# Kernel tuning notes

Measured on AMD Instinct MI355X. Metric: run time of the kernel, lower is better.

The kernel has to match this reference:

```python
import jax, jax.numpy as jnp
import numpy as np

EPS = 1e-12

def _l2norm(x):
    # F.normalize(p=2, dim=1) with eps clamp on the norm
    n = jnp.linalg.norm(x, axis=1, keepdims=True)
    return x / jnp.maximum(n, EPS)

def _xavier_uniform(key, shape, gain=1.414):
    fan_in, fan_out = shape[-1], shape[0]
    a = gain * np.sqrt(6.0 / (fan_in + fan_out))
    return jax.random.uniform(key, shape, jnp.float32, -a, a)

def setup_inputs() -> dict:
    NUM_ENT, NUM_REL, D, E, B = 100000, 500, 512, 150000, 4096
    key = jax.random.key(0)
    ks = jax.random.split(key, 12)
    heads = jax.random.randint(ks[0], (B, 1), 0, NUM_ENT)
    rels  = jax.random.randint(ks[1], (B, 1), 0, NUM_REL)
    tails = jax.random.randint(ks[2], (B, 1), 0, NUM_ENT)
    triples = jnp.concatenate([heads, rels, tails], axis=1)           # [B,3]
    node_list = jax.random.randint(ks[3], (2, E), 0, NUM_ENT)          # [2,E] (src,dst)
    edge_list = jax.random.randint(ks[4], (E,), 0, NUM_REL)            # [E] relation per edge
    return {
        "triples": triples,
        "node_list": node_list,
        "edge_list": edge_list,
        "ent_emb_init": jax.random.normal(ks[5], (NUM_ENT, D), jnp.float32),
        "rel_emb_init": jax.random.normal(ks[6], (NUM_REL, D), jnp.float32),
        "W_1": _xavier_uniform(ks[7], (D, D)),
        "W_a": _xavier_uniform(ks[8], (1, D)),
        "g_0": _xavier_uniform(ks[9], (1, D)),
        "W_E": _xavier_uniform(ks[10], (D, D)),
        "W_R": _xavier_uniform(ks[11], (D, D)),
    }

def reference(triples, node_list, edge_list, ent_emb_init, rel_emb_init,
              W_1, W_a, g_0, W_E, W_R):
    num_ent = ent_emb_init.shape[0]
    e0 = _l2norm(ent_emb_init)                      # normalized entity table [N,D]
    src, dst = node_list[0], node_list[1]
    h_i = e0[src]                                   # [E,D]
    h_j = e0[dst]                                   # [E,D]
    g_k = rel_emb_init[edge_list]                   # [E,D]

    # c_ijk = W_1 @ (h_j*g_k)^T  -> kept edge-major as [E,D]
    c = (h_j * g_k) @ W_1.T                         # [E,D]
    a = -jax.nn.leaky_relu((h_i * jnp.tanh(c)) @ W_a[0], 0.2)   # [E]
    c_base = (h_i * g_0) @ W_1.T                    # [E,D]
    a_base = -jax.nn.leaky_relu((h_i * jnp.tanh(c_base)) @ W_a[0], 0.2)  # [E]

    a_exp = jnp.exp(a)                              # [E]
    ab_exp = jnp.exp(a_base)                        # [E]

    # segment-softmax denominator: sum of edge exps per source node + baseline term
    a_exp_sum = jax.ops.segment_sum(a_exp[:, None], src, num_segments=num_ent)  # [N,1]
    # baseline exp depends only on src node -> duplicate scatter-set writes identical values
    ab_sorted = jnp.zeros_like(a_exp_sum).at[src].set(ab_exp[:, None])           # [N,1]
    denom = ab_sorted + a_exp_sum
    denom = jnp.where(denom == 0.0, EPS, denom)

    # weighted scatter-aggregate of messages (dropout omitted: eval-mode identity)
    ac = a_exp[:, None] * c                         # [E,D]
    ac_base = ab_exp[:, None] * c_base              # [E,D]
    a_new = jax.ops.segment_sum(ac, src, num_segments=num_ent)                   # [N,D]
    ab_new = jnp.zeros_like(a_new).at[src].set(ac_base)                          # [N,D]

    h_prime = jax.nn.elu((ab_new + a_new) / denom)  # [N,D]
    ent_new = _l2norm(e0 @ W_E + h_prime)           # [N,D]
    rel_new = rel_emb_init @ W_R                    # [R,D]

    head = ent_new[triples[:, 0]][:, None, :]       # [B,1,D]
    rel  = rel_new[triples[:, 1]][:, None, :]       # [B,1,D]
    tail = ent_new[triples[:, 2]][:, None, :]       # [B,1,D]
    return jnp.concatenate([head, rel, tail], axis=1)  # [B,3,D]
```

## Files before the change

kernel.cpp:

```cpp
#include <hip/hip_runtime.h>
#include <cmath>


#define DDIM 512
#define MAXM 65536
#define GBM 128
#define GBN 128

typedef __attribute__((ext_vector_type(8))) short short8;
typedef __attribute__((ext_vector_type(4))) float fv4;
typedef unsigned short u16;

__device__ __forceinline__ float elu1(float x) { return x > 0.f ? x : expm1f(x); }
__device__ __forceinline__ float sexp(float x) {
    float lr = x >= 0.f ? x : 0.2f * x;
    return expf(-lr);
}
__device__ __forceinline__ u16 f2bf(float x) {
    unsigned u = __float_as_uint(x);
    u += 0x7FFFu + ((u >> 16) & 1u);
    return (u16)(u >> 16);
}
__device__ __forceinline__ float bf2f(u16 h) {
    return __uint_as_float((unsigned)h << 16);
}
__device__ __forceinline__ void cvt8(const float* v, short8& h8, short8& l8) {
    #pragma unroll
    for (int i = 0; i < 8; i++) {
        u16 h = f2bf(v[i]);
        h8[i] = (short)h;
        l8[i] = (short)f2bf(v[i] - bf2f(h));
    }
}
__device__ __forceinline__ void gld16(const void* g, void* l) {
    __builtin_amdgcn_global_load_lds(
        (const __attribute__((address_space(1))) unsigned int*)g,
        (__attribute__((address_space(3))) unsigned int*)l,
        16, 0, 0);
}

__global__ __launch_bounds__(128)
void invnorm_sel_kernel(const float* __restrict__ emb, const int* __restrict__ slotNode,
                        const int* __restrict__ rowsL, const int* __restrict__ dstIdx,
                        const int* __restrict__ Mdev, int NS, float* __restrict__ invN)
{
    __shared__ float ws2[2];
    int total = NS + min(MAXM, *Mdev);
    int t = threadIdx.x;
    for (int q = blockIdx.x; q < total; q += gridDim.x) {
        int n = (q < NS) ? slotNode[q] : dstIdx[rowsL[q - NS]];
        float4 v = *(const float4*)(emb + (size_t)n * DDIM + t * 4);
        float s = v.x*v.x + v.y*v.y + v.z*v.z + v.w*v.w;
        #pragma unroll
        for (int off = 32; off > 0; off >>= 1) s += __shfl_down(s, off);
        if ((t & 63) == 0) ws2[t >> 6] = s;
        __syncthreads();
        if (t == 0) invN[n] = 1.f / fmaxf(sqrtf(ws2[0] + ws2[1]), 1e-12f);
        __syncthreads();
    }
}

__global__ __launch_bounds__(128)
void l2norm_kernel(float* __restrict__ data)
{
    int r = blockIdx.x, t = threadIdx.x;
    size_t o = (size_t)r * DDIM + t * 4;
    float4 v = *(const float4*)(data + o);
    float s = v.x*v.x + v.y*v.y + v.z*v.z + v.w*v.w;
    #pragma unroll
    for (int off = 32; off > 0; off >>= 1) s += __shfl_down(s, off);
    __shared__ float ws2[2];
    if ((t & 63) == 0) ws2[t >> 6] = s;
    __syncthreads();
    float inv = 1.f / fmaxf(sqrtf(ws2[0] + ws2[1]), 1e-12f);
    *(float4*)(data + o) = make_float4(v.x*inv, v.y*inv, v.z*inv, v.w*inv);
}

__global__ __launch_bounds__(256)
void transpose512_kernel(const float* __restrict__ in, float* __restrict__ out)
{
    __shared__ float tile[32][33];
    int bx = blockIdx.x & 15, by = blockIdx.x >> 4;
    int x = threadIdx.x & 31, y0 = (threadIdx.x >> 5) * 4;
    #pragma unroll
    for (int i = 0; i < 4; i++)
        tile[y0 + i][x] = in[(size_t)(by * 32 + y0 + i) * 512 + bx * 32 + x];
    __syncthreads();
    #pragma unroll
    for (int i = 0; i < 4; i++)
        out[(size_t)(bx * 32 + y0 + i) * 512 + by * 32 + x] = tile[x][y0 + i];
}

__global__ void hist_kernel(const int* __restrict__ src, int* __restrict__ cnt, int E)
{
    int e = blockIdx.x * 256 + threadIdx.x;
    if (e < E) atomicAdd(&cnt[src[e]], 1);
}

__global__ __launch_bounds__(1024)
void scan1_kernel(const int* __restrict__ in, int* __restrict__ out,
                  int* __restrict__ blockTot, int n)
{
    __shared__ int sh[1024];
    int t = threadIdx.x;
    int i = blockIdx.x * 1024 + t;
    int v = (i < n) ? in[i] : 0;
    sh[t] = v;
    __syncthreads();
    for (int off = 1; off < 1024; off <<= 1) {
        int x = (t >= off) ? sh[t - off] : 0;
        __syncthreads();
        sh[t] += x;
        __syncthreads();
    }
    if (i < n) out[i] = sh[t] - v;
    if (t == 1023) blockTot[blockIdx.x] = sh[1023];
}

__global__ __launch_bounds__(1024)
void scan2_kernel(const int* __restrict__ blockTot, int* __restrict__ blockOff,
                  int* __restrict__ outLast, int G)
{
    __shared__ int sh[1024];
    int t = threadIdx.x;
    int v = (t < G) ? blockTot[t] : 0;
    sh[t] = v;
    __syncthreads();
    for (int off = 1; off < 1024; off <<= 1) {
        int x = (t >= off) ? sh[t - off] : 0;
        __syncthreads();
        sh[t] += x;
        __syncthreads();
    }
    if (t < G) blockOff[t] = sh[t] - v;
    if (t == 1023) *outLast = sh[1023];
}

__global__ __launch_bounds__(1024)
void scan3_kernel(int* __restrict__ out, const int* __restrict__ blockOff, int n)
{
    int i = blockIdx.x * 1024 + threadIdx.x;
    if (i < n) out[i] += blockOff[blockIdx.x];
}

__global__ void bucket_kernel(const int* __restrict__ src, int* __restrict__ cursor,
                              int* __restrict__ edge_ids, int E)
{
    int e = blockIdx.x * 256 + threadIdx.x;
    if (e < E) { int p = atomicAdd(&cursor[src[e]], 1); edge_ids[p] = e; }
}

__global__ void slotdeg_kernel(const int* __restrict__ triples, const int* __restrict__ rowSt,
                               int* __restrict__ slotNode, int* __restrict__ deg, int NS)
{
    int r = blockIdx.x * 256 + threadIdx.x;
    if (r < NS) {
        int b = r >> 1, p = (r & 1) * 2;
        int n = triples[b * 3 + p];
        slotNode[r] = n;
        deg[r] = rowSt[n + 1] - rowSt[n];
    }
}

__global__ void fill_rows_kernel(const int* __restrict__ slotNode, const int* __restrict__ rowSt,
                                 const int* __restrict__ edgeIds, const int* __restrict__ slotOff,
                                 int* __restrict__ rows, int* __restrict__ srcL, int NS)
{
    int r = blockIdx.x * 256 + threadIdx.x;
    if (r >= NS) return;
    int n = slotNode[r];
    int gs = rowSt[n], d = rowSt[n + 1] - gs, mo = slotOff[r];
    for (int j = 0; j < d && mo + j < MAXM; j++) {
        rows[mo + j] = edgeIds[gs + j];
        srcL[mo + j] = n;
    }
}

__global__ __launch_bounds__(256)
void afrag_dense_kernel(const float* __restrict__ in, int rows,
                        u16* __restrict__ hi, u16* __restrict__ lo)
{
    int nt = ((rows + 127) >> 7) << 3;
    int wid = threadIdx.x >> 6, lane = threadIdx.x & 63;
    int l15 = lane & 15, seg = (lane >> 4) * 8;
    for (int rt = blockIdx.x * 4 + wid; rt < nt; rt += gridDim.x * 4) {
        int r = min(rt * 16 + l15, rows - 1);
        const float* p = in + (size_t)r * DDIM + seg;
        size_t base = (size_t)rt * 8192 + (size_t)lane * 8;
        #pragma unroll 4
        for (int kt = 0; kt < 16; kt++) {
            float4 x0 = *(const float4*)(p + kt * 32);
            float4 x1 = *(const float4*)(p + kt * 32 + 4);
            float v[8] = {x0.x, x0.y, x0.z, x0.w, x1.x, x1.y, x1.z, x1.w};
            short8 h8, l8; cvt8(v, h8, l8);
            *(short8*)(hi + base + (size_t)kt * 512) = h8;
            *(short8*)(lo + base + (size_t)kt * 512) = l8;
        }
    }
}

__global__ __launch_bounds__(256)
void afrag_edge_kernel(const float* __restrict__ entEmb, const float* __restrict__ invN,
                       const float* __restrict__ relEmb, const int* __restrict__ rowsL,
                       const int* __restrict__ dstIdx, const int* __restrict__ relIdx,
                       const int* __restrict__ Mdev,
                       u16* __restrict__ hi, u16* __restrict__ lo)
{
    int M = max(1, min(MAXM, *Mdev));
    int nt = ((M + 127) >> 7) << 3;
    int wid = threadIdx.x >> 6, lane = threadIdx.x & 63;
    int l15 = lane & 15, seg = (lane >> 4) * 8;
    for (int rt = blockIdx.x * 4 + wid; rt < nt; rt += gridDim.x * 4) {
        int m = min(rt * 16 + l15, M - 1);
        int e = rowsL[m];
        int dn = dstIdx[e], rl = relIdx[e];
        float sc = invN[dn];
        const float* ep = entEmb + (size_t)dn * DDIM + seg;
        const float* rp = relEmb + (size_t)rl * DDIM + seg;
        size_t base = (size_t)rt * 8192 + (size_t)lane * 8;
        #pragma unroll 4
        for (int kt = 0; kt < 16; kt++) {
            float4 x0 = *(const float4*)(ep + kt * 32);
            float4 x1 = *(const float4*)(ep + kt * 32 + 4);
            float4 y0 = *(const float4*)(rp + kt * 32);
            float4 y1 = *(const float4*)(rp + kt * 32 + 4);
            float v[8] = {sc*x0.x*y0.x, sc*x0.y*y0.y, sc*x0.z*y0.z, sc*x0.w*y0.w,
                          sc*x1.x*y1.x, sc*x1.y*y1.y, sc*x1.z*y1.z, sc*x1.w*y1.w};
            short8 h8, l8; cvt8(v, h8, l8);
            *(short8*)(hi + base + (size_t)kt * 512) = h8;
            *(short8*)(lo + base + (size_t)kt * 512) = l8;
        }
    }
}

__global__ __launch_bounds__(256)
void afrag_slot_kernel(const float* __restrict__ entEmb, const float* __restrict__ invN,
                       const float* __restrict__ g0, const int* __restrict__ slotNode,
                       int NS, u16* __restrict__ s1h, u16* __restrict__ s1l,
                       u16* __restrict__ s3h, u16* __restrict__ s3l)
{
    int nt = ((NS + 127) >> 7) << 3;
    int wid = threadIdx.x >> 6, lane = threadIdx.x & 63;
    int l15 = lane & 15, seg = (lane >> 4) * 8;
    for (int rt = blockIdx.x * 4 + wid; rt < nt; rt += gridDim.x * 4) {
        int r = min(rt * 16 + l15, NS - 1);
        int n = slotNode[r];
        float sc = invN[n];
        const float* ep = entEmb + (size_t)n * DDIM + seg;
        const float* gp = g0 + seg;
        size_t base = (size_t)rt * 8192 + (size_t)lane * 8;
        #pragma unroll 2
        for (int kt = 0; kt < 16; kt++) {
            float4 x0 = *(const float4*)(ep + kt * 32);
            float4 x1 = *(const float4*)(ep + kt * 32 + 4);
            float4 y0 = *(const float4*)(gp + kt * 32);
            float4 y1 = *(const float4*)(gp + kt * 32 + 4);
            float v3[8] = {sc*x0.x, sc*x0.y, sc*x0.z, sc*x0.w,
                           sc*x1.x, sc*x1.y, sc*x1.z, sc*x1.w};
            float v1[8] = {v3[0]*y0.x, v3[1]*y0.y, v3[2]*y0.z, v3[3]*y0.w,
                           v3[4]*y1.x, v3[5]*y1.y, v3[6]*y1.z, v3[7]*y1.w};
            short8 h8, l8;
            cvt8(v3, h8, l8);
            *(short8*)(s3h + base + (size_t)kt * 512) = h8;
            *(short8*)(s3l + base + (size_t)kt * 512) = l8;
            cvt8(v1, h8, l8);
            *(short8*)(s1h + base + (size_t)kt * 512) = h8;
            *(short8*)(s1l + base + (size_t)kt * 512) = l8;
        }
    }
}

template<int EPI, bool DEVM>
__global__ __launch_bounds__(256)
void gemm_frag_k(const u16* __restrict__ Ahi, const u16* __restrict__ Alo,
                 const u16* __restrict__ Bhi, const u16* __restrict__ Blo,
                 const float* __restrict__ entEmb, const float* __restrict__ invNorm,
                 const int* __restrict__ srcMap, const float* __restrict__ Wa,
                 float* __restrict__ scoreOut, const float* __restrict__ invDenom,
                 const float* __restrict__ Hadd, float* __restrict__ Cout,
                 int Mhost, const int* __restrict__ Mdev)
{
    __shared__ __align__(1024) u16 lds[2][32 * 512];

    int M = DEVM ? max(1, min(MAXM, *Mdev)) : Mhost;
    int lane = threadIdx.x & 63, wid = threadIdx.x >> 6;
    int waveM = wid >> 1, waveN = wid & 1;
    int quad = lane >> 4, l15 = lane & 15;
    int n0 = blockIdx.y * GBN;

    const u16* gcls = (wid == 0) ? Ahi : (wid == 1) ? Alo : (wid == 2) ? Bhi : Blo;
    int ldsChunk0 = wid * 8;

    for (int mt = blockIdx.x; mt * GBM < M; mt += gridDim.x) {
        int m0 = mt * GBM;
        int rowBase = (wid < 2) ? (m0 >> 4) : (n0 >> 4);
        const u16* src0 = gcls + (size_t)rowBase * 8192 + (size_t)lane * 8;

        fv4 acc[4][4];
        #pragma unroll
        for (int i = 0; i < 4; i++)
            #pragma unroll
            for (int j = 0; j < 4; j++) acc[i][j] = fv4{0.f, 0.f, 0.f, 0.f};

        int cur = 0;
        #pragma unroll
        for (int q = 0; q < 8; q++)
            gld16(src0 + (size_t)q * 8192, &lds[0][(ldsChunk0 + q) * 512]);
        __syncthreads();

        for (int kt = 0; kt < 16; kt++) {
            if (kt < 15) {
                size_t go = (size_t)(kt + 1) * 512;
                #pragma unroll
                for (int q = 0; q < 8; q++)
                    gld16(src0 + (size_t)q * 8192 + go,
                          &lds[cur ^ 1][(ldsChunk0 + q) * 512]);
            }
            const u16* buf = &lds[cur][0];
            short8 aH[4], aL[4], bH[4], bL[4];
            #pragma unroll
            for (int i = 0; i < 4; i++) {
                aH[i] = *(const short8*)&buf[(waveM * 4 + i) * 512 + lane * 8];
                aL[i] = *(const short8*)&buf[(8 + waveM * 4 + i) * 512 + lane * 8];
                bH[i] = *(const short8*)&buf[(16 + waveN * 4 + i) * 512 + lane * 8];
                bL[i] = *(const short8*)&buf[(24 + waveN * 4 + i) * 512 + lane * 8];
            }
            #pragma unroll
            for (int i = 0; i < 4; i++)
                #pragma unroll
                for (int j = 0; j < 4; j++) {
                    acc[i][j] = __builtin_amdgcn_mfma_f32_16x16x32_bf16(aH[i], bH[j], acc[i][j], 0, 0, 0);
                    acc[i][j] = __builtin_amdgcn_mfma_f32_16x16x32_bf16(aH[i], bL[j], acc[i][j], 0, 0, 0);
                    acc[i][j] = __builtin_amdgcn_mfma_f32_16x16x32_bf16(aL[i], bH[j], acc[i][j], 0, 0, 0);
                }
            __syncthreads();
            cur ^= 1;
        }

        if (EPI == 1) {
            #pragma unroll
            for (int i = 0; i < 4; i++) {
                #pragma unroll
                for (int reg = 0; reg < 4; reg++) {
                    int gm = m0 + waveM * 64 + i * 16 + quad * 4 + reg;
                    bool valid = gm < M;
                    int gmc = valid ? gm : 0;
                    int srcn = srcMap[gmc];
                    float invs = invNorm[srcn];
                    float s = 0.f;
                    #pragma unroll
                    for (int j = 0; j < 4; j++) {
                        int col = n0 + waveN * 64 + j * 16 + l15;
                        float hv = entEmb[(size_t)srcn * DDIM + col];
                        float wv = Wa[col];
                        s += tanhf(acc[i][j][reg]) * hv * wv;
                    }
                    s *= invs;
                    s += __shfl_xor(s, 8); s += __shfl_xor(s, 4);
                    s += __shfl_xor(s, 2); s += __shfl_xor(s, 1);
                    if (l15 == 0 && valid) atomicAdd(scoreOut + gm, s);
                }
            }
        } else {
            #pragma unroll
            for (int i = 0; i < 4; i++) {
                #pragma unroll
                for (int reg = 0; reg < 4; reg++) {
                    int gm = m0 + waveM * 64 + i * 16 + quad * 4 + reg;
                    if (gm >= M) continue;
                    float idv = (EPI == 2) ? invDenom[gm] : 0.f;
                    #pragma unroll
                    for (int j = 0; j < 4; j++) {
                        int col = n0 + waveN * 64 + j * 16 + l15;
                        size_t o = (size_t)gm * DDIM + col;
                        float v = acc[i][j][reg];
                        if (EPI == 2) v = elu1(v * idv);
                        else if (EPI == 3) v += Hadd[o];
                        Cout[o] = v;
                    }
                }
            }
        }
    }
}

__global__ __launch_bounds__(128)
void build_p_kernel(const float* __restrict__ entEmb, const float* __restrict__ invNorm,
                    const float* __restrict__ relEmb, const float* __restrict__ g0,
                    const int* __restrict__ slotNode, const int* __restrict__ rowSt,
                    const int* __restrict__ edgeIds, const int* __restrict__ dstIdx,
                    const int* __restrict__ relIdx, const int* __restrict__ slotOff,
                    const float* __restrict__ scoreE, const float* __restrict__ scoreS,
                    float* __restrict__ P, float* __restrict__ invDenom)
{
    int r = blockIdx.x, t = threadIdx.x;
    int n = slotNode[r];
    int gs = rowSt[n], d = rowSt[n + 1] - gs;
    size_t po = (size_t)r * DDIM + t * 4;
    if (d == 0) {
        *(float4*)(P + po) = make_float4(0.f, 0.f, 0.f, 0.f);
        if (t == 0) invDenom[r] = 1.f;
        return;
    }
    int mo = slotOff[r];
    float ab = sexp(scoreS[r]);
    float sc = ab * invNorm[n];
    float4 ev = *(const float4*)(entEmb + (size_t)n * DDIM + t * 4);
    float4 gv = *(const float4*)(g0 + t * 4);
    float4 acc = make_float4(sc*ev.x*gv.x, sc*ev.y*gv.y, sc*ev.z*gv.z, sc*ev.w*gv.w);
    float denom = ab;
    for (int j = 0; j < d; j++) {
        if (mo + j >= MAXM) break;
        int e = edgeIds[gs + j];
        float ae = sexp(scoreE[mo + j]);
        int dn = dstIdx[e], rl = relIdx[e];
        float s = ae * invNorm[dn];
        float4 dv = *(const float4*)(entEmb + (size_t)dn * DDIM + t * 4);
        float4 rv = *(const float4*)(relEmb + (size_t)rl * DDIM + t * 4);
        acc.x = fmaf(s, dv.x*rv.x, acc.x);
        acc.y = fmaf(s, dv.y*rv.y, acc.y);
        acc.z = fmaf(s, dv.z*rv.z, acc.z);
        acc.w = fmaf(s, dv.w*rv.w, acc.w);
        denom += ae;
    }
    *(float4*)(P + po) = acc;
    if (t == 0) invDenom[r] = 1.f / denom;
}

__global__ __launch_bounds__(128)
void gather_out_kernel(const int* __restrict__ triples, const float* __restrict__ ENT,
                       const float* __restrict__ relnew, float* __restrict__ out)
{
    int r = blockIdx.x;
    int b = r / 3, j = r - b * 3;
    const float* srow;
    if (j == 1) srow = relnew + (size_t)triples[r] * DDIM;
    else        srow = ENT + (size_t)(b * 2 + (j == 2 ? 1 : 0)) * DDIM;
    int t = threadIdx.x * 4;
    *(float4*)(out + (size_t)r * DDIM + t) = *(const float4*)(srow + t);
}

extern "C" void kernel_launch(void* const* d_in, const int* in_sizes, int n_in,
                              void* d_out, int out_size, void* d_ws, size_t ws_size,
                              hipStream_t stream)
{
    const int*   triples = (const int*)  d_in[0];
    const int*   nodes   = (const int*)  d_in[1];
    const int*   edges   = (const int*)  d_in[2];
    const float* entEmb  = (const float*)d_in[3];
    const float* relEmb  = (const float*)d_in[4];
    const float* W1      = (const float*)d_in[5];
    const float* Wa      = (const float*)d_in[6];
    const float* g0      = (const float*)d_in[7];
    const float* WE      = (const float*)d_in[8];
    const float* WR      = (const float*)d_in[9];

    const int B  = in_sizes[0] / 3;
    const int E  = in_sizes[2];
    const int N  = in_sizes[3] / DDIM;
    const int R  = in_sizes[4] / DDIM;
    const int NS = 2 * B;
    const int* srcIdx = nodes;
    const int* dstIdx = nodes + E;

    char* ws = (char*)d_ws;
    size_t off = 0;
    auto carve = [&](size_t bytes) -> void* {
        void* p = ws + off;
        off = (off + bytes + 255) & ~(size_t)255;
        return p;
    };
    const int NS128 = ((NS + 127) / 128) * 128;
    const int R128  = ((R + 127) / 128) * 128;
    float* P        = (float*)carve((size_t)NS * DDIM * 4);
    float* H        = (float*)carve((size_t)NS * DDIM * 4);
    float* ENT      = (float*)carve((size_t)NS * DDIM * 4);
    float* relnew   = (float*)carve((size_t)R * DDIM * 4);
    float* WET      = (float*)carve((size_t)DDIM * DDIM * 4);
    float* WRT      = (float*)carve((size_t)DDIM * DDIM * 4);
    float* invNorm  = (float*)carve((size_t)N * 4);
    float* score_e  = (float*)carve((size_t)MAXM * 4);
    float* score_s  = (float*)carve((size_t)NS * 4);
    float* invDen   = (float*)carve((size_t)NS * 4);
    int*   cnt      = (int*)carve((size_t)N * 4);
    int*   rowSt    = (int*)carve((size_t)(N + 1) * 4);
    int*   cursor   = (int*)carve((size_t)N * 4);
    int*   edgeIds  = (int*)carve((size_t)E * 4);
    int*   slotNode = (int*)carve((size_t)NS * 4);
    int*   deg      = (int*)carve((size_t)NS * 4);
    int*   slotOff  = (int*)carve((size_t)(NS + 1) * 4);
    int*   rowsL    = (int*)carve((size_t)MAXM * 4);
    int*   srcL     = (int*)carve((size_t)MAXM * 4);
    int*   blockTot = (int*)carve((size_t)1024 * 4);
    int*   blockOff = (int*)carve((size_t)1024 * 4);
    u16* AeH = (u16*)carve((size_t)MAXM * DDIM * 2);
    u16* AeL = (u16*)carve((size_t)MAXM * DDIM * 2);
    u16* As1H = (u16*)carve((size_t)NS128 * DDIM * 2);
    u16* As1L = (u16*)carve((size_t)NS128 * DDIM * 2);
    u16* As3H = (u16*)carve((size_t)NS128 * DDIM * 2);
    u16* As3L = (u16*)carve((size_t)NS128 * DDIM * 2);
    u16* ApH = (u16*)carve((size_t)NS128 * DDIM * 2);
    u16* ApL = (u16*)carve((size_t)NS128 * DDIM * 2);
    u16* ArH = (u16*)carve((size_t)R128 * DDIM * 2);
    u16* ArL = (u16*)carve((size_t)R128 * DDIM * 2);
    u16* W1H = (u16*)carve((size_t)DDIM * DDIM * 2);
    u16* W1L = (u16*)carve((size_t)DDIM * DDIM * 2);
    u16* WEH = (u16*)carve((size_t)DDIM * DDIM * 2);
    u16* WEL = (u16*)carve((size_t)DDIM * DDIM * 2);
    u16* WRH = (u16*)carve((size_t)DDIM * DDIM * 2);
    u16* WRL = (u16*)carve((size_t)DDIM * DDIM * 2);
    (void)ws_size; (void)n_in; (void)out_size;

    auto scan = [&](const int* in, int* out, int n) {
        int G = (n + 1023) / 1024;
        scan1_kernel<<<G, 1024, 0, stream>>>(in, out, blockTot, n);
        scan2_kernel<<<1, 1024, 0, stream>>>(blockTot, blockOff, out + n, G);
        scan3_kernel<<<G, 1024, 0, stream>>>(out, blockOff, n);
    };

    hipMemsetAsync(cnt, 0, (size_t)N * 4, stream);
    hist_kernel<<<(E + 255) / 256, 256, 0, stream>>>(srcIdx, cnt, E);
    scan(cnt, rowSt, N);
    hipMemcpyAsync(cursor, rowSt, (size_t)N * 4, hipMemcpyDeviceToDevice, stream);
    bucket_kernel<<<(E + 255) / 256, 256, 0, stream>>>(srcIdx, cursor, edgeIds, E);

    slotdeg_kernel<<<(NS + 255) / 256, 256, 0, stream>>>(triples, rowSt, slotNode, deg, NS);
    scan(deg, slotOff, NS);
    fill_rows_kernel<<<(NS + 255) / 256, 256, 0, stream>>>(slotNode, rowSt, edgeIds,
                                                           slotOff, rowsL, srcL, NS);
    const int* Mdev = slotOff + NS;

    invnorm_sel_kernel<<<4096, 128, 0, stream>>>(entEmb, slotNode, rowsL, dstIdx,
                                                 Mdev, NS, invNorm);

    transpose512_kernel<<<256, 256, 0, stream>>>(WE, WET);
    transpose512_kernel<<<256, 256, 0, stream>>>(WR, WRT);
    afrag_dense_kernel<<<8, 256, 0, stream>>>(W1, DDIM, W1H, W1L);
    afrag_dense_kernel<<<8, 256, 0, stream>>>(WET, DDIM, WEH, WEL);
    afrag_dense_kernel<<<8, 256, 0, stream>>>(WRT, DDIM, WRH, WRL);

    afrag_edge_kernel<<<128, 256, 0, stream>>>(entEmb, invNorm, relEmb, rowsL,
                                               dstIdx, edges, Mdev, AeH, AeL);
    afrag_slot_kernel<<<128, 256, 0, stream>>>(entEmb, invNorm, g0, slotNode, NS,
                                               As1H, As1L, As3H, As3L);

    hipMemsetAsync(score_e, 0, (size_t)MAXM * 4, stream);
    hipMemsetAsync(score_s, 0, (size_t)NS * 4, stream);
    dim3 gEdge(128, DDIM / GBN);
    gemm_frag_k<1, true><<<gEdge, 256, 0, stream>>>(
        AeH, AeL, W1H, W1L, entEmb, invNorm, srcL, Wa,
        score_e, nullptr, nullptr, nullptr, 0, Mdev);
    dim3 gSlot((NS + GBM - 1) / GBM, DDIM / GBN);
    gemm_frag_k<1, false><<<gSlot, 256, 0, stream>>>(
        As1H, As1L, W1H, W1L, entEmb, invNorm, slotNode, Wa,
        score_s, nullptr, nullptr, nullptr, NS, nullptr);

    build_p_kernel<<<NS, 128, 0, stream>>>(entEmb, invNorm, relEmb, g0, slotNode,
                                           rowSt, edgeIds, dstIdx, edges, slotOff,
                                           score_e, score_s, P, invDen);

    afrag_dense_kernel<<<128, 256, 0, stream>>>(P, NS, ApH, ApL);
    gemm_frag_k<2, false><<<gSlot, 256, 0, stream>>>(
        ApH, ApL, W1H, W1L, entEmb, invNorm, nullptr, nullptr,
        nullptr, invDen, nullptr, H, NS, nullptr);

    gemm_frag_k<3, false><<<gSlot, 256, 0, stream>>>(
        As3H, As3L, WEH, WEL, entEmb, invNorm, nullptr, nullptr,
        nullptr, nullptr, H, ENT, NS, nullptr);
    l2norm_kernel<<<NS, 128, 0, stream>>>(ENT);

    afrag_dense_kernel<<<8, 256, 0, stream>>>(relEmb, R, ArH, ArL);
    dim3 gRel((R + GBM - 1) / GBM, DDIM / GBN);
    gemm_frag_k<0, false><<<gRel, 256, 0, stream>>>(
        ArH, ArL, WRH, WRL, entEmb, invNorm, nullptr, nullptr,
        nullptr, nullptr, nullptr, relnew, R, nullptr);

    gather_out_kernel<<<B * 3, 128, 0, stream>>>(triples, ENT, relnew, (float*)d_out);
}
```

Measured before the change: 555.5 us.

## Fuse preprocessing kernels and merge the two slot GEMMs into one pass

Combines many small launches. The scan add now also fills the cursor, replacing the memcpy. Bucket and slotdeg run as one kernel. The weight transposes and fragment conversions become one wfrag kernel, and the edge and slot fragment builders become one. build_p now writes bf16 hi/lo fragments directly instead of an fp32 P buffer. The P@W1 GEMM with ELU and the e0@WE GEMM are fused into one 32-step K loop, with ELU applied to the accumulator mid-loop, so the H buffer goes away. This cuts launch overhead and intermediate global traffic. The costs are uncoalesced strided reads for the transposed weights and the loss of the max(1,M) guard.

Result: faster. 496.4 us (-10.6%).

```diff
diff --git a/kernel.cpp b/kernel.cpp
--- a/kernel.cpp
+++ b/kernel.cpp
@@ -8,6 +8,7 @@
 #define GBN 128
 
 typedef __attribute__((ext_vector_type(8))) short short8;
+typedef __attribute__((ext_vector_type(4))) short short4v;
 typedef __attribute__((ext_vector_type(4))) float fv4;
 typedef unsigned short u16;
 
@@ -76,21 +77,6 @@
     *(float4*)(data + o) = make_float4(v.x*inv, v.y*inv, v.z*inv, v.w*inv);
 }
 
-__global__ __launch_bounds__(256)
-void transpose512_kernel(const float* __restrict__ in, float* __restrict__ out)
-{
-    __shared__ float tile[32][33];
-    int bx = blockIdx.x & 15, by = blockIdx.x >> 4;
-    int x = threadIdx.x & 31, y0 = (threadIdx.x >> 5) * 4;
-    #pragma unroll
-    for (int i = 0; i < 4; i++)
-        tile[y0 + i][x] = in[(size_t)(by * 32 + y0 + i) * 512 + bx * 32 + x];
-    __syncthreads();
-    #pragma unroll
-    for (int i = 0; i < 4; i++)
-        out[(size_t)(bx * 32 + y0 + i) * 512 + by * 32 + x] = tile[x][y0 + i];
-}
-
 __global__ void hist_kernel(const int* __restrict__ src, int* __restrict__ cnt, int E)
 {
     int e = blockIdx.x * 256 + threadIdx.x;
@@ -137,24 +123,26 @@
 }
 
 __global__ __launch_bounds__(1024)
-void scan3_kernel(int* __restrict__ out, const int* __restrict__ blockOff, int n)
+void scan3_dual_kernel(int* __restrict__ out, const int* __restrict__ blockOff,
+                       int* __restrict__ out2, int n)
 {
     int i = blockIdx.x * 1024 + threadIdx.x;
-    if (i < n) out[i] += blockOff[blockIdx.x];
-}
-
-__global__ void bucket_kernel(const int* __restrict__ src, int* __restrict__ cursor,
-                              int* __restrict__ edge_ids, int E)
-{
-    int e = blockIdx.x * 256 + threadIdx.x;
-    if (e < E) { int p = atomicAdd(&cursor[src[e]], 1); edge_ids[p] = e; }
-}
-
-__global__ void slotdeg_kernel(const int* __restrict__ triples, const int* __restrict__ rowSt,
-                               int* __restrict__ slotNode, int* __restrict__ deg, int NS)
-{
-    int r = blockIdx.x * 256 + threadIdx.x;
-    if (r < NS) {
+    if (i < n) {
+        int v = out[i] + blockOff[blockIdx.x];
+        out[i] = v;
+        if (out2) out2[i] = v;
+    }
+}
+
+__global__ void bucket_slotdeg_kernel(const int* __restrict__ src, int* __restrict__ cursor,
+                                      int* __restrict__ edge_ids, int E,
+                                      const int* __restrict__ triples, const int* __restrict__ rowSt,
+                                      int* __restrict__ slotNode, int* __restrict__ deg, int NS)
+{
+    int i = blockIdx.x * 256 + threadIdx.x;
+    if (i < E) { int p = atomicAdd(&cursor[src[i]], 1); edge_ids[p] = i; }
+    int r = i - E;
+    if (r >= 0 && r < NS) {
         int b = r >> 1, p = (r & 1) * 2;
         int n = triples[b * 3 + p];
         slotNode[r] = n;
@@ -176,22 +164,44 @@
     }
 }
 
+
 __global__ __launch_bounds__(256)
-void afrag_dense_kernel(const float* __restrict__ in, int rows,
-                        u16* __restrict__ hi, u16* __restrict__ lo)
-{
+void wfrag_kernel(const float* __restrict__ W1, const float* __restrict__ WE,
+                  const float* __restrict__ WR, const float* __restrict__ relEmb,
+                  int R,
+                  u16* __restrict__ W1H, u16* __restrict__ W1L,
+                  u16* __restrict__ WEH, u16* __restrict__ WEL,
+                  u16* __restrict__ WRH, u16* __restrict__ WRL,
+                  u16* __restrict__ ArH, u16* __restrict__ ArL)
+{
+    int mat = blockIdx.y;
+    const float* src = (mat == 0) ? W1 : (mat == 1) ? WE : (mat == 2) ? WR : relEmb;
+    u16* hi = (mat == 0) ? W1H : (mat == 1) ? WEH : (mat == 2) ? WRH : ArH;
+    u16* lo = (mat == 0) ? W1L : (mat == 1) ? WEL : (mat == 2) ? WRL : ArL;
+    bool tr = (mat == 1 || mat == 2);
+    int rows = (mat == 3) ? R : DDIM;
+
     int nt = ((rows + 127) >> 7) << 3;
     int wid = threadIdx.x >> 6, lane = threadIdx.x & 63;
     int l15 = lane & 15, seg = (lane >> 4) * 8;
     for (int rt = blockIdx.x * 4 + wid; rt < nt; rt += gridDim.x * 4) {
         int r = min(rt * 16 + l15, rows - 1);
-        const float* p = in + (size_t)r * DDIM + seg;
         size_t base = (size_t)rt * 8192 + (size_t)lane * 8;
-        #pragma unroll 4
+        #pragma unroll 2
         for (int kt = 0; kt < 16; kt++) {
-            float4 x0 = *(const float4*)(p + kt * 32);
-            float4 x1 = *(const float4*)(p + kt * 32 + 4);
-            float v[8] = {x0.x, x0.y, x0.z, x0.w, x1.x, x1.y, x1.z, x1.w};
+            float v[8];
+            if (!tr) {
+                const float* p = src + (size_t)r * DDIM + seg + kt * 32;
+                float4 x0 = *(const float4*)p;
+                float4 x1 = *(const float4*)(p + 4);
+                v[0]=x0.x; v[1]=x0.y; v[2]=x0.z; v[3]=x0.w;
+                v[4]=x1.x; v[5]=x1.y; v[6]=x1.z; v[7]=x1.w;
+            } else {
+                int k0 = kt * 32 + seg;
+                #pragma unroll
+                for (int i = 0; i < 8; i++)
+                    v[i] = src[(size_t)(k0 + i) * DDIM + r];
+            }
             short8 h8, l8; cvt8(v, h8, l8);
             *(short8*)(hi + base + (size_t)kt * 512) = h8;
             *(short8*)(lo + base + (size_t)kt * 512) = l8;
@@ -200,72 +210,70 @@
 }
 
 __global__ __launch_bounds__(256)
-void afrag_edge_kernel(const float* __restrict__ entEmb, const float* __restrict__ invN,
-                       const float* __restrict__ relEmb, const int* __restrict__ rowsL,
-                       const int* __restrict__ dstIdx, const int* __restrict__ relIdx,
-                       const int* __restrict__ Mdev,
-                       u16* __restrict__ hi, u16* __restrict__ lo)
-{
-    int M = max(1, min(MAXM, *Mdev));
-    int nt = ((M + 127) >> 7) << 3;
+void afrag_es_kernel(const float* __restrict__ entEmb, const float* __restrict__ invN,
+                     const float* __restrict__ relEmb, const float* __restrict__ g0,
+                     const int* __restrict__ rowsL, const int* __restrict__ dstIdx,
+                     const int* __restrict__ relIdx, const int* __restrict__ slotNode,
+                     const int* __restrict__ Mdev, int NS,
+                     u16* __restrict__ AeH, u16* __restrict__ AeL,
+                     u16* __restrict__ As1H, u16* __restrict__ As1L,
+                     u16* __restrict__ As3H, u16* __restrict__ As3L)
+{
+    int M = min(MAXM, *Mdev);
+    int ntE = ((M + 127) >> 7) << 3;
+    int ntS = ((NS + 127) >> 7) << 3;
+    int total = ntE + ntS;
     int wid = threadIdx.x >> 6, lane = threadIdx.x & 63;
     int l15 = lane & 15, seg = (lane >> 4) * 8;
-    for (int rt = blockIdx.x * 4 + wid; rt < nt; rt += gridDim.x * 4) {
-        int m = min(rt * 16 + l15, M - 1);
-        int e = rowsL[m];
-        int dn = dstIdx[e], rl = relIdx[e];
-        float sc = invN[dn];
-        const float* ep = entEmb + (size_t)dn * DDIM + seg;
-        const float* rp = relEmb + (size_t)rl * DDIM + seg;
-        size_t base = (size_t)rt * 8192 + (size_t)lane * 8;
-        #pragma unroll 4
-        for (int kt = 0; kt < 16; kt++) {
-            float4 x0 = *(const float4*)(ep + kt * 32);
-            float4 x1 = *(const float4*)(ep + kt * 32 + 4);
-            float4 y0 = *(const float4*)(rp + kt * 32);
-            float4 y1 = *(const float4*)(rp + kt * 32 + 4);
-            float v[8] = {sc*x0.x*y0.x, sc*x0.y*y0.y, sc*x0.z*y0.z, sc*x0.w*y0.w,
-                          sc*x1.x*y1.x, sc*x1.y*y1.y, sc*x1.z*y1.z, sc*x1.w*y1.w};
-            short8 h8, l8; cvt8(v, h8, l8);
-            *(short8*)(hi + base + (size_t)kt * 512) = h8;
-            *(short8*)(lo + base + (size_t)kt * 512) = l8;
-        }
-    }
-}
-
-__global__ __launch_bounds__(256)
-void afrag_slot_kernel(const float* __restrict__ entEmb, const float* __restrict__ invN,
-                       const float* __restrict__ g0, const int* __restrict__ slotNode,
-                       int NS, u16* __restrict__ s1h, u16* __restrict__ s1l,
-                       u16* __restrict__ s3h, u16* __restrict__ s3l)
-{
-    int nt = ((NS + 127) >> 7) << 3;
-    int wid = threadIdx.x >> 6, lane = threadIdx.x & 63;
-    int l15 = lane & 15, seg = (lane >> 4) * 8;
-    for (int rt = blockIdx.x * 4 + wid; rt < nt; rt += gridDim.x * 4) {
-        int r = min(rt * 16 + l15, NS - 1);
-        int n = slotNode[r];
-        float sc = invN[n];
-        const float* ep = entEmb + (size_t)n * DDIM + seg;
-        const float* gp = g0 + seg;
-        size_t base = (size_t)rt * 8192 + (size_t)lane * 8;
-        #pragma unroll 2
-        for (int kt = 0; kt < 16; kt++) {
-            float4 x0 = *(const float4*)(ep + kt * 32);
-            float4 x1 = *(const float4*)(ep + kt * 32 + 4);
-            float4 y0 = *(const float4*)(gp + kt * 32);
-            float4 y1 = *(const float4*)(gp + kt * 32 + 4);
-            float v3[8] = {sc*x0.x, sc*x0.y, sc*x0.z, sc*x0.w,
-                           sc*x1.x, sc*x1.y, sc*x1.z, sc*x1.w};
-            float v1[8] = {v3[0]*y0.x, v3[1]*y0.y, v3[2]*y0.z, v3[3]*y0.w,
-                           v3[4]*y1.x, v3[5]*y1.y, v3[6]*y1.z, v3[7]*y1.w};
-            short8 h8, l8;
-            cvt8(v3, h8, l8);
-            *(short8*)(s3h + base + (size_t)kt * 512) = h8;
-            *(short8*)(s3l + base + (size_t)kt * 512) = l8;
-            cvt8(v1, h8, l8);
-            *(short8*)(s1h + base + (size_t)kt * 512) = h8;
-            *(short8*)(s1l + base + (size_t)kt * 512) = l8;
+
+    for (int g = blockIdx.x * 4 + wid; g < total; g += gridDim.x * 4) {
+        if (g < ntE) {
+            int rt = g;
+            int m = min(rt * 16 + l15, M - 1);
+            int e = rowsL[m];
+            int dn = dstIdx[e], rl = relIdx[e];
+            float sc = invN[dn];
+            const float* ep = entEmb + (size_t)dn * DDIM + seg;
+            const float* rp = relEmb + (size_t)rl * DDIM + seg;
+            size_t base = (size_t)rt * 8192 + (size_t)lane * 8;
+            #pragma unroll 4
+            for (int kt = 0; kt < 16; kt++) {
+                float4 x0 = *(const float4*)(ep + kt * 32);
+                float4 x1 = *(const float4*)(ep + kt * 32 + 4);
+                float4 y0 = *(const float4*)(rp + kt * 32);
+                float4 y1 = *(const float4*)(rp + kt * 32 + 4);
+                float v[8] = {sc*x0.x*y0.x, sc*x0.y*y0.y, sc*x0.z*y0.z, sc*x0.w*y0.w,
+                              sc*x1.x*y1.x, sc*x1.y*y1.y, sc*x1.z*y1.z, sc*x1.w*y1.w};
+                short8 h8, l8; cvt8(v, h8, l8);
+                *(short8*)(AeH + base + (size_t)kt * 512) = h8;
+                *(short8*)(AeL + base + (size_t)kt * 512) = l8;
+            }
+        } else {
+            int rt = g - ntE;
+            int r = min(rt * 16 + l15, NS - 1);
+            int n = slotNode[r];
+            float sc = invN[n];
+            const float* ep = entEmb + (size_t)n * DDIM + seg;
+            const float* gp = g0 + seg;
+            size_t base = (size_t)rt * 8192 + (size_t)lane * 8;
+            #pragma unroll 2
+            for (int kt = 0; kt < 16; kt++) {
+                float4 x0 = *(const float4*)(ep + kt * 32);
+                float4 x1 = *(const float4*)(ep + kt * 32 + 4);
+                float4 y0 = *(const float4*)(gp + kt * 32);
+                float4 y1 = *(const float4*)(gp + kt * 32 + 4);
+                float v3[8] = {sc*x0.x, sc*x0.y, sc*x0.z, sc*x0.w,
+                               sc*x1.x, sc*x1.y, sc*x1.z, sc*x1.w};
+                float v1[8] = {v3[0]*y0.x, v3[1]*y0.y, v3[2]*y0.z, v3[3]*y0.w,
+                               v3[4]*y1.x, v3[5]*y1.y, v3[6]*y1.z, v3[7]*y1.w};
+                short8 h8, l8;
+                cvt8(v3, h8, l8);
+                *(short8*)(As3H + base + (size_t)kt * 512) = h8;
+                *(short8*)(As3L + base + (size_t)kt * 512) = l8;
+                cvt8(v1, h8, l8);
+                *(short8*)(As1H + base + (size_t)kt * 512) = h8;
+                *(short8*)(As1L + base + (size_t)kt * 512) = l8;
+            }
         }
     }
 }
@@ -274,27 +282,34 @@
 __global__ __launch_bounds__(256)
 void gemm_frag_k(const u16* __restrict__ Ahi, const u16* __restrict__ Alo,
                  const u16* __restrict__ Bhi, const u16* __restrict__ Blo,
+                 const u16* __restrict__ A2hi, const u16* __restrict__ A2lo,
+                 const u16* __restrict__ B2hi, const u16* __restrict__ B2lo,
                  const float* __restrict__ entEmb, const float* __restrict__ invNorm,
                  const int* __restrict__ srcMap, const float* __restrict__ Wa,
                  float* __restrict__ scoreOut, const float* __restrict__ invDenom,
-                 const float* __restrict__ Hadd, float* __restrict__ Cout,
+                 float* __restrict__ Cout,
                  int Mhost, const int* __restrict__ Mdev)
 {
     __shared__ __align__(1024) u16 lds[2][32 * 512];
 
-    int M = DEVM ? max(1, min(MAXM, *Mdev)) : Mhost;
+    int M = DEVM ? min(MAXM, *Mdev) : Mhost;
     int lane = threadIdx.x & 63, wid = threadIdx.x >> 6;
     int waveM = wid >> 1, waveN = wid & 1;
     int quad = lane >> 4, l15 = lane & 15;
     int n0 = blockIdx.y * GBN;
 
-    const u16* gcls = (wid == 0) ? Ahi : (wid == 1) ? Alo : (wid == 2) ? Bhi : Blo;
+    const u16* g1 = (wid == 0) ? Ahi : (wid == 1) ? Alo : (wid == 2) ? Bhi : Blo;
+    const u16* g2 = (EPI == 4)
+        ? ((wid == 0) ? A2hi : (wid == 1) ? A2lo : (wid == 2) ? B2hi : B2lo)
+        : nullptr;
     int ldsChunk0 = wid * 8;
+    const int NKK = (EPI == 4) ? 32 : 16;
 
     for (int mt = blockIdx.x; mt * GBM < M; mt += gridDim.x) {
         int m0 = mt * GBM;
         int rowBase = (wid < 2) ? (m0 >> 4) : (n0 >> 4);
-        const u16* src0 = gcls + (size_t)rowBase * 8192 + (size_t)lane * 8;
+        const u16* s1 = g1 + (size_t)rowBase * 8192 + (size_t)lane * 8;
+        const u16* s2 = (EPI == 4) ? g2 + (size_t)rowBase * 8192 + (size_t)lane * 8 : nullptr;
 
         fv4 acc[4][4];
         #pragma unroll
@@ -305,15 +320,17 @@
         int cur = 0;
         #pragma unroll
         for (int q = 0; q < 8; q++)
-            gld16(src0 + (size_t)q * 8192, &lds[0][(ldsChunk0 + q) * 512]);
+            gld16(s1 + (size_t)q * 8192, &lds[0][(ldsChunk0 + q) * 512]);
         __syncthreads();
 
-        for (int kt = 0; kt < 16; kt++) {
-            if (kt < 15) {
-                size_t go = (size_t)(kt + 1) * 512;
+        for (int kk = 0; kk < NKK; kk++) {
+            int kn = kk + 1;
+            if (kn < NKK) {
+                const u16* sp = (EPI == 4 && kn >= 16) ? s2 : s1;
+                size_t go = (size_t)(kn & 15) * 512;
                 #pragma unroll
                 for (int q = 0; q < 8; q++)
-                    gld16(src0 + (size_t)q * 8192 + go,
+                    gld16(sp + (size_t)q * 8192 + go,
                           &lds[cur ^ 1][(ldsChunk0 + q) * 512]);
             }
             const u16* buf = &lds[cur][0];
@@ -333,6 +350,18 @@
                     acc[i][j] = __builtin_amdgcn_mfma_f32_16x16x32_bf16(aH[i], bL[j], acc[i][j], 0, 0, 0);
                     acc[i][j] = __builtin_amdgcn_mfma_f32_16x16x32_bf16(aL[i], bH[j], acc[i][j], 0, 0, 0);
                 }
+            if (EPI == 4 && kk == 15) {
+                #pragma unroll
+                for (int i = 0; i < 4; i++)
+                    #pragma unroll
+                    for (int reg = 0; reg < 4; reg++) {
+                        int gm = m0 + waveM * 64 + i * 16 + quad * 4 + reg;
+                        float idv = invDenom[min(gm, M - 1)];
+                        #pragma unroll
+                        for (int j = 0; j < 4; j++)
+                            acc[i][j][reg] = elu1(acc[i][j][reg] * idv);
+                    }
+            }
             __syncthreads();
             cur ^= 1;
         }
@@ -368,15 +397,10 @@
                 for (int reg = 0; reg < 4; reg++) {
                     int gm = m0 + waveM * 64 + i * 16 + quad * 4 + reg;
                     if (gm >= M) continue;
-                    float idv = (EPI == 2) ? invDenom[gm] : 0.f;
                     #pragma unroll
                     for (int j = 0; j < 4; j++) {
                         int col = n0 + waveN * 64 + j * 16 + l15;
-                        size_t o = (size_t)gm * DDIM + col;
-                        float v = acc[i][j][reg];
-                        if (EPI == 2) v = elu1(v * idv);
-                        else if (EPI == 3) v += Hadd[o];
-                        Cout[o] = v;
+                        Cout[(size_t)gm * DDIM + col] = acc[i][j][reg];
                     }
                 }
             }
@@ -391,40 +415,56 @@
                     const int* __restrict__ edgeIds, const int* __restrict__ dstIdx,
                     const int* __restrict__ relIdx, const int* __restrict__ slotOff,
                     const float* __restrict__ scoreE, const float* __restrict__ scoreS,
-                    float* __restrict__ P, float* __restrict__ invDenom)
+                    int NS,
+                    u16* __restrict__ ApH, u16* __restrict__ ApL,
+                    float* __restrict__ invDenom)
 {
     int r = blockIdx.x, t = threadIdx.x;
-    int n = slotNode[r];
-    int gs = rowSt[n], d = rowSt[n + 1] - gs;
-    size_t po = (size_t)r * DDIM + t * 4;
-    if (d == 0) {
-        *(float4*)(P + po) = make_float4(0.f, 0.f, 0.f, 0.f);
-        if (t == 0) invDenom[r] = 1.f;
-        return;
-    }
-    int mo = slotOff[r];
-    float ab = sexp(scoreS[r]);
-    float sc = ab * invNorm[n];
-    float4 ev = *(const float4*)(entEmb + (size_t)n * DDIM + t * 4);
-    float4 gv = *(const float4*)(g0 + t * 4);
-    float4 acc = make_float4(sc*ev.x*gv.x, sc*ev.y*gv.y, sc*ev.z*gv.z, sc*ev.w*gv.w);
-    float denom = ab;
-    for (int j = 0; j < d; j++) {
-        if (mo + j >= MAXM) break;
-        int e = edgeIds[gs + j];
-        float ae = sexp(scoreE[mo + j]);
-        int dn = dstIdx[e], rl = relIdx[e];
-        float s = ae * invNorm[dn];
-        float4 dv = *(const float4*)(entEmb + (size_t)dn * DDIM + t * 4);
-        float4 rv = *(const float4*)(relEmb + (size_t)rl * DDIM + t * 4);
-        acc.x = fmaf(s, dv.x*rv.x, acc.x);
-        acc.y = fmaf(s, dv.y*rv.y, acc.y);
-        acc.z = fmaf(s, dv.z*rv.z, acc.z);
-        acc.w = fmaf(s, dv.w*rv.w, acc.w);
-        denom += ae;
-    }
-    *(float4*)(P + po) = acc;
-    if (t == 0) invDenom[r] = 1.f / denom;
+    float4 acc = make_float4(0.f, 0.f, 0.f, 0.f);
+    float dInv = 1.f;
+    if (r < NS) {
+        int n = slotNode[r];
+        int gs = rowSt[n], d = rowSt[n + 1] - gs;
+        if (d > 0) {
+            int mo = slotOff[r];
+            float ab = sexp(scoreS[r]);
+            float sc = ab * invNorm[n];
+            float4 ev = *(const float4*)(entEmb + (size_t)n * DDIM + t * 4);
+            float4 gv = *(const float4*)(g0 + t * 4);
+            acc = make_float4(sc*ev.x*gv.x, sc*ev.y*gv.y, sc*ev.z*gv.z, sc*ev.w*gv.w);
+            float denom = ab;
+            for (int j = 0; j < d; j++) {
+                if (mo + j >= MAXM) break;
+                int e = edgeIds[gs + j];
+                float ae = sexp(scoreE[mo + j]);
+                int dn = dstIdx[e], rl = relIdx[e];
+                float s = ae * invNorm[dn];
+                float4 dv = *(const float4*)(entEmb + (size_t)dn * DDIM + t * 4);
+                float4 rv = *(const float4*)(relEmb + (size_t)rl * DDIM + t * 4);
+                acc.x = fmaf(s, dv.x*rv.x, acc.x);
+                acc.y = fmaf(s, dv.y*rv.y, acc.y);
+                acc.z = fmaf(s, dv.z*rv.z, acc.z);
+                acc.w = fmaf(s, dv.w*rv.w, acc.w);
+                denom += ae;
+            }
+            dInv = 1.f / denom;
+        }
+    }
+    int kt = t >> 3;
+    int lane = (r & 15) + 16 * ((t >> 1) & 3);
+    int j0 = (t & 1) * 4;
+    size_t fo = (size_t)(r >> 4) * 8192 + (size_t)kt * 512 + (size_t)lane * 8 + j0;
+    float v[4] = {acc.x, acc.y, acc.z, acc.w};
+    short4v h4, l4;
+    #pragma unroll
+    for (int i = 0; i < 4; i++) {
+        u16 h = f2bf(v[i]);
+        h4[i] = (short)h;
+        l4[i] = (short)f2bf(v[i] - bf2f(h));
+    }
+    *(short4v*)(ApH + fo) = h4;
+    *(short4v*)(ApL + fo) = l4;
+    if (t == 0 && r < NS) invDenom[r] = dInv;
 }
 
 __global__ __launch_bounds__(128)
@@ -472,15 +512,12 @@
     };
     const int NS128 = ((NS + 127) / 128) * 128;
     const int R128  = ((R + 127) / 128) * 128;
-    float* P        = (float*)carve((size_t)NS * DDIM * 4);
-    float* H        = (float*)carve((size_t)NS * DDIM * 4);
     float* ENT      = (float*)carve((size_t)NS * DDIM * 4);
     float* relnew   = (float*)carve((size_t)R * DDIM * 4);
-    float* WET      = (float*)carve((size_t)DDIM * DDIM * 4);
-    float* WRT      = (float*)carve((size_t)DDIM * DDIM * 4);
     float* invNorm  = (float*)carve((size_t)N * 4);
-    float* score_e  = (float*)carve((size_t)MAXM * 4);
-    float* score_s  = (float*)carve((size_t)NS * 4);
+    float* scoreAll = (float*)carve((size_t)(MAXM + NS) * 4);
+    float* score_e  = scoreAll;
+    float* score_s  = scoreAll + MAXM;
     float* invDen   = (float*)carve((size_t)NS * 4);
     int*   cnt      = (int*)carve((size_t)N * 4);
     int*   rowSt    = (int*)carve((size_t)(N + 1) * 4);
@@ -493,39 +530,40 @@
     int*   srcL     = (int*)carve((size_t)MAXM * 4);
     int*   blockTot = (int*)carve((size_t)1024 * 4);
     int*   blockOff = (int*)carve((size_t)1024 * 4);
-    u16* AeH = (u16*)carve((size_t)MAXM * DDIM * 2);
-    u16* AeL = (u16*)carve((size_t)MAXM * DDIM * 2);
+    u16* AeH  = (u16*)carve((size_t)MAXM * DDIM * 2);
+    u16* AeL  = (u16*)carve((size_t)MAXM * DDIM * 2);
     u16* As1H = (u16*)carve((size_t)NS128 * DDIM * 2);
     u16* As1L = (u16*)carve((size_t)NS128 * DDIM * 2);
     u16* As3H = (u16*)carve((size_t)NS128 * DDIM * 2);
     u16* As3L = (u16*)carve((size_t)NS128 * DDIM * 2);
-    u16* ApH = (u16*)carve((size_t)NS128 * DDIM * 2);
-    u16* ApL = (u16*)carve((size_t)NS128 * DDIM * 2);
-    u16* ArH = (u16*)carve((size_t)R128 * DDIM * 2);
-    u16* ArL = (u16*)carve((size_t)R128 * DDIM * 2);
-    u16* W1H = (u16*)carve((size_t)DDIM * DDIM * 2);
-    u16* W1L = (u16*)carve((size_t)DDIM * DDIM * 2);
-    u16* WEH = (u16*)carve((size_t)DDIM * DDIM * 2);
-    u16* WEL = (u16*)carve((size_t)DDIM * DDIM * 2);
-    u16* WRH = (u16*)carve((size_t)DDIM * DDIM * 2);
-    u16* WRL = (u16*)carve((size_t)DDIM * DDIM * 2);
+    u16* ApH  = (u16*)carve((size_t)NS128 * DDIM * 2);
+    u16* ApL  = (u16*)carve((size_t)NS128 * DDIM * 2);
+    u16* ArH  = (u16*)carve((size_t)R128 * DDIM * 2);
+    u16* ArL  = (u16*)carve((size_t)R128 * DDIM * 2);
+    u16* W1H  = (u16*)carve((size_t)DDIM * DDIM * 2);
+    u16* W1L  = (u16*)carve((size_t)DDIM * DDIM * 2);
+    u16* WEH  = (u16*)carve((size_t)DDIM * DDIM * 2);
+    u16* WEL  = (u16*)carve((size_t)DDIM * DDIM * 2);
+    u16* WRH  = (u16*)carve((size_t)DDIM * DDIM * 2);
+    u16* WRL  = (u16*)carve((size_t)DDIM * DDIM * 2);
     (void)ws_size; (void)n_in; (void)out_size;
-
-    auto scan = [&](const int* in, int* out, int n) {
-        int G = (n + 1023) / 1024;
-        scan1_kernel<<<G, 1024, 0, stream>>>(in, out, blockTot, n);
-        scan2_kernel<<<1, 1024, 0, stream>>>(blockTot, blockOff, out + n, G);
-        scan3_kernel<<<G, 1024, 0, stream>>>(out, blockOff, n);
-    };
 
     hipMemsetAsync(cnt, 0, (size_t)N * 4, stream);
     hist_kernel<<<(E + 255) / 256, 256, 0, stream>>>(srcIdx, cnt, E);
-    scan(cnt, rowSt, N);
-    hipMemcpyAsync(cursor, rowSt, (size_t)N * 4, hipMemcpyDeviceToDevice, stream);
-    bucket_kernel<<<(E + 255) / 256, 256, 0, stream>>>(srcIdx, cursor, edgeIds, E);
-
-    slotdeg_kernel<<<(NS + 255) / 256, 256, 0, stream>>>(triples, rowSt, slotNode, deg, NS);
-    scan(deg, slotOff, NS);
+    {
+        int G = (N + 1023) / 1024;
+        scan1_kernel<<<G, 1024, 0, stream>>>(cnt, rowSt, blockTot, N);
+        scan2_kernel<<<1, 1024, 0, stream>>>(blockTot, blockOff, rowSt + N, G);
+        scan3_dual_kernel<<<G, 1024, 0, stream>>>(rowSt, blockOff, cursor, N);
+    }
+    bucket_slotdeg_kernel<<<(E + NS + 255) / 256, 256, 0, stream>>>(
+        srcIdx, cursor, edgeIds, E, triples, rowSt, slotNode, deg, NS);
+    {
+        int G = (NS + 1023) / 1024;
+        scan1_kernel<<<G, 1024, 0, stream>>>(deg, slotOff, blockTot, NS);
+        scan2_kernel<<<1, 1024, 0, stream>>>(blockTot, blockOff, slotOff + NS, G);
+        scan3_dual_kernel<<<G, 1024, 0, stream>>>(slotOff, blockOff, nullptr, NS);
+    }
     fill_rows_kernel<<<(NS + 255) / 256, 256, 0, stream>>>(slotNode, rowSt, edgeIds,
                                                            slotOff, rowsL, srcL, NS);
     const int* Mdev = slotOff + NS;
@@ -533,47 +571,37 @@
     invnorm_sel_kernel<<<4096, 128, 0, stream>>>(entEmb, slotNode, rowsL, dstIdx,
                                                  Mdev, NS, invNorm);
 
-    transpose512_kernel<<<256, 256, 0, stream>>>(WE, WET);
-    transpose512_kernel<<<256, 256, 0, stream>>>(WR, WRT);
-    afrag_dense_kernel<<<8, 256, 0, stream>>>(W1, DDIM, W1H, W1L);
-    afrag_dense_kernel<<<8, 256, 0, stream>>>(WET, DDIM, WEH, WEL);
-    afrag_dense_kernel<<<8, 256, 0, stream>>>(WRT, DDIM, WRH, WRL);
-
-    afrag_edge_kernel<<<128, 256, 0, stream>>>(entEmb, invNorm, relEmb, rowsL,
-                                               dstIdx, edges, Mdev, AeH, AeL);
-    afrag_slot_kernel<<<128, 256, 0, stream>>>(entEmb, invNorm, g0, slotNode, NS,
-                                               As1H, As1L, As3H, As3L);
-
-    hipMemsetAsync(score_e, 0, (size_t)MAXM * 4, stream);
-    hipMemsetAsync(score_s, 0, (size_t)NS * 4, stream);
+    wfrag_kernel<<<dim3(8, 4), 256, 0, stream>>>(W1, WE, WR, relEmb, R,
+                                                 W1H, W1L, WEH, WEL, WRH, WRL, ArH, ArL);
+
+    afrag_es_kernel<<<256, 256, 0, stream>>>(entEmb, invNorm, relEmb, g0,
+                                             rowsL, dstIdx, edges, slotNode,
+                                             Mdev, NS,
+                                             AeH, AeL, As1H, As1L, As3H, As3L);
+
+    hipMemsetAsync(scoreAll, 0, (size_t)(MAXM + NS) * 4, stream);
     dim3 gEdge(128, DDIM / GBN);
     gemm_frag_k<1, true><<<gEdge, 256, 0, stream>>>(
-        AeH, AeL, W1H, W1L, entEmb, invNorm, srcL, Wa,
-        score_e, nullptr, nullptr, nullptr, 0, Mdev);
+        AeH, AeL, W1H, W1L, nullptr, nullptr, nullptr, nullptr,
+        entEmb, invNorm, srcL, Wa, score_e, nullptr, nullptr, 0, Mdev);
     dim3 gSlot((NS + GBM - 1) / GBM, DDIM / GBN);
     gemm_frag_k<1, false><<<gSlot, 256, 0, stream>>>(
-        As1H, As1L, W1H, W1L, entEmb, invNorm, slotNode, Wa,
-        score_s, nullptr, nullptr, nullptr, NS, nullptr);
-
-    build_p_kernel<<<NS, 128, 0, stream>>>(entEmb, invNorm, relEmb, g0, slotNode,
-                                           rowSt, edgeIds, dstIdx, edges, slotOff,
-                                           score_e, score_s, P, invDen);
-
-    afrag_dense_kernel<<<128, 256, 0, stream>>>(P, NS, ApH, ApL);
-    gemm_frag_k<2, false><<<gSlot, 256, 0, stream>>>(
-        ApH, ApL, W1H, W1L, entEmb, invNorm, nullptr, nullptr,
-        nullptr, invDen, nullptr, H, NS, nullptr);
-
-    gemm_frag_k<3, false><<<gSlot, 256, 0, stream>>>(
-        As3H, As3L, WEH, WEL, entEmb, invNorm, nullptr, nullptr,
-        nullptr, nullptr, H, ENT, NS, nullptr);
+        As1H, As1L, W1H, W1L, nullptr, nullptr, nullptr, nullptr,
+        entEmb, invNorm, slotNode, Wa, score_s, nullptr, nullptr, NS, nullptr);
+
+    build_p_kernel<<<NS128, 128, 0, stream>>>(entEmb, invNorm, relEmb, g0, slotNode,
+                                              rowSt, edgeIds, dstIdx, edges, slotOff,
+                                              score_e, score_s, NS, ApH, ApL, invDen);
+
+    gemm_frag_k<4, false><<<gSlot, 256, 0, stream>>>(
+        ApH, ApL, W1H, W1L, As3H, As3L, WEH, WEL,
+        entEmb, invNorm, nullptr, nullptr, nullptr, invDen, ENT, NS, nullptr);
     l2norm_kernel<<<NS, 128, 0, stream>>>(ENT);
 
-    afrag_dense_kernel<<<8, 256, 0, stream>>>(relEmb, R, ArH, ArL);
     dim3 gRel((R + GBM - 1) / GBM, DDIM / GBN);
     gemm_frag_k<0, false><<<gRel, 256, 0, stream>>>(
-        ArH, ArL, WRH, WRL, entEmb, invNorm, nullptr, nullptr,
-        nullptr, nullptr, nullptr, relnew, R, nullptr);
+        ArH, ArL, WRH, WRL, nullptr, nullptr, nullptr, nullptr,
+        entEmb, invNorm, nullptr, nullptr, nullptr, nullptr, relnew, R, nullptr);
 
     gather_out_kernel<<<B * 3, 128, 0, stream>>>(triples, ENT, relnew, (float*)d_out);
 }
```
